# Performance work log

Measured on AMD Instinct MI355X. Metric: run time of the kernel, lower is better.

The kernel has to match this reference:

```python
import jax, jax.numpy as jnp
import numpy as np

NHEAD = 8; DM = 512; DFF = 2048; L = 4; S = 1024; NTOK = 51; MLP = 256; CLASSES = 7
GH = 3; GHID = 64; GCLS = 5; ALPHA = 0.2
HD = DM // NHEAD

_ADJ = np.array([[0,1,0,0,0],[1,1,1,1,0],[1,0,1,0,1],[1,0,0,1,1],[0,0,1,1,1]], dtype=np.int32)


def setup_inputs():
    key = jax.random.key(0)
    ks = jax.random.split(key, 24)
    r = lambda k, s, sc=0.05: jax.random.normal(k, s, jnp.float32) * sc
    return {
        'x': jax.random.normal(ks[0], (5, S, NTOK), jnp.float32),
        'adj': jnp.asarray(_ADJ),
        'W_enc': r(ks[1], (NTOK, DM)), 'b_enc': jnp.zeros((DM,), jnp.float32),
        'cls_tok': r(ks[2], (1, 1, DM)),
        'pos_emb': r(ks[3], (S + 1, DM)),
        'Wq': r(ks[4], (L, DM, DM)), 'bq': jnp.zeros((L, DM), jnp.float32),
        'Wk': r(ks[5], (L, DM, DM)), 'bk': jnp.zeros((L, DM), jnp.float32),
        'Wv': r(ks[6], (L, DM, DM)), 'bv': jnp.zeros((L, DM), jnp.float32),
        'Wo': r(ks[7], (L, DM, DM)), 'bo': jnp.zeros((L, DM), jnp.float32),
        'W1': r(ks[8], (L, DM, DFF)), 'b1': jnp.zeros((L, DFF), jnp.float32),
        'W2': r(ks[9], (L, DFF, DM)), 'b2': jnp.zeros((L, DM), jnp.float32),
        'g1': jnp.ones((L, DM), jnp.float32), 'be1': jnp.zeros((L, DM), jnp.float32),
        'g2': jnp.ones((L, DM), jnp.float32), 'be2': jnp.zeros((L, DM), jnp.float32),
        'Wd1': r(ks[10], (DM, MLP)), 'bd1': jnp.zeros((MLP,), jnp.float32),
        'Wd2': r(ks[11], (MLP, CLASSES)), 'bd2': jnp.zeros((CLASSES,), jnp.float32),
        'Wg': r(ks[12], (GH, 3, GHID), 0.3), 'ag': r(ks[13], (GH, 2 * GHID), 0.3),
        'Wgo': r(ks[14], (GH * GHID, GCLS), 0.3), 'ago': r(ks[15], (2 * GCLS,), 0.3),
    }


def _layernorm(x, g, b, eps=1e-5):
    m = x.mean(-1, keepdims=True)
    v = ((x - m) ** 2).mean(-1, keepdims=True)
    return (x - m) * jax.lax.rsqrt(v + eps) * g + b


def _gat_attn_layer(h_in, W, a, mask):
    # standard pyGAT GraphAttentionLayer: e_ij = LeakyReLU(a1.h_i + a2.h_j)
    F = W.shape[1]
    h = h_in @ W                                                    # [N, F]
    e = jax.nn.leaky_relu((h @ a[:F])[:, None] + (h @ a[F:])[None, :], ALPHA)
    att = jax.nn.softmax(jnp.where(mask, e, -9e15), axis=-1)        # adjacency-masked softmax
    return att @ h


def _gat(xg, mask, Wg, ag, Wgo, ago):
    # xg: [5 nodes, 3 feats]; GH attention heads concatenated, then output layer
    heads = jax.vmap(lambda W, a: jax.nn.elu(_gat_attn_layer(xg, W, a, mask)))(Wg, ag)  # [GH,5,GHID]
    hcat = jnp.transpose(heads, (1, 0, 2)).reshape(xg.shape[0], GH * GHID)
    out = jax.nn.elu(_gat_attn_layer(hcat, Wgo, ago, mask))         # [5, GCLS]
    return jax.nn.log_softmax(out, axis=1)


def _forward(x, adj, params):
    (W_enc, b_enc, cls_tok, pos_emb, Wq, bq, Wk, bk, Wv, bv, Wo, bo,
     W1, b1, W2, b2, g1, be1, g2, be2, Wd1, bd1, Wd2, bd2, Wg, ag, Wgo, ago) = params
    mask = adj > 0
    # --- batched GAT: the source loops over T timesteps x 5 feature groups; here fully vectorized ---
    # x[:, :, :15] : batch(=5 nodes) x T x 15 -> [T*5groups, 5 nodes, 3]
    xg = x[:, :, :15].reshape(5, S, 5, 3)
    xg = jnp.transpose(xg, (1, 2, 0, 3)).reshape(S * 5, 5, 3)
    gat_out = jax.vmap(lambda g: _gat(g, mask, Wg, ag, Wgo, ago))(xg)
    gat_out = gat_out.reshape(S, 5, 5, GCLS)                        # [T, group, node, class]
    # --- transformer branch (eval mode: dropout = identity) ---
    h = x @ W_enc + b_enc                                           # [5, S, DM]
    h = jnp.concatenate([jnp.broadcast_to(cls_tok, (5, 1, DM)), h], axis=1)
    h = h + pos_emb[None]
    for i in range(L):
        q = (h @ Wq[i] + bq[i]).reshape(5, S + 1, NHEAD, HD)
        k = (h @ Wk[i] + bk[i]).reshape(5, S + 1, NHEAD, HD)
        v = (h @ Wv[i] + bv[i]).reshape(5, S + 1, NHEAD, HD)
        sc = jnp.einsum('bthd,bshd->bhts', q, k) / jnp.sqrt(jnp.float32(HD))
        att = jax.nn.softmax(sc, axis=-1)
        o = jnp.einsum('bhts,bshd->bthd', att, v).reshape(5, S + 1, DM) @ Wo[i] + bo[i]
        h = _layernorm(h + o, g1[i], be1[i])
        f = jax.nn.relu(h @ W1[i] + b1[i]) @ W2[i] + b2[i]
        h = _layernorm(h + f, g2[i], be2[i])
    cls = h[:, 0, :]                                                # lambda: x[:, 0, :]
    out = (cls @ Wd1 + bd1) @ Wd2 + bd2                             # no activation between dense layers (as in source)
    return out, gat_out


def reference(x, adj, W_enc, b_enc, cls_tok, pos_emb, Wq, bq, Wk, bk, Wv, bv, Wo, bo, W1, b1, W2, b2, g1, be1, g2, be2, Wd1, bd1, Wd2, bd2, Wg, ag, Wgo, ago):
    params = (W_enc, b_enc, cls_tok, pos_emb, Wq, bq, Wk, bk, Wv, bv, Wo, bo,
              W1, b1, W2, b2, g1, be1, g2, be2, Wd1, bd1, Wd2, bd2, Wg, ag, Wgo, ago)
    return _forward(x, adj, params)
```

## Files before the change

### kernel.cpp

```cpp
#include <hip/hip_runtime.h>
#include <hip/hip_bf16.h>
#include <math.h>

#define NBATCH 5
#define SEQ    1024
#define T      1025
#define ROWS   (NBATCH * T)
#define MP     5248
#define DM     512
#define DFF    2048
#define NHEAD  8
#define HD     64
#define NTOK   51
#define MLPDIM 256
#define NCLS   7
#define GH     3
#define GHID   64
#define GCLS   5
#define NGRAPH (SEQ * 5)
#define QKVN   1536
#define TPAD   1088

typedef __attribute__((ext_vector_type(8))) short bf16x8;
typedef __attribute__((ext_vector_type(4))) float f32x4;

#define GM_AS(p)  ((const __attribute__((address_space(1))) void*)(p))
#define LDS_AS(p) ((__attribute__((address_space(3))) void*)(p))

__device__ __forceinline__ unsigned short f2bf(float f) {
    unsigned int u = __float_as_uint(f);
    unsigned int r = (u + 0x7FFFu + ((u >> 16) & 1u)) >> 16;
    return (unsigned short)r;
}
__device__ __forceinline__ float bf2f(unsigned short u) {
    return __uint_as_float((unsigned int)u << 16);
}

__global__ __launch_bounds__(256) void wconv_kernel(
    const float* __restrict__ W, unsigned short* __restrict__ Wt, int K, int N,
    long dstride)
{
    const float* Wm = W + (size_t)blockIdx.z * K * N;
    unsigned short* Wo = Wt + (size_t)blockIdx.z * dstride;
    __shared__ float tile[32][33];
    int bx = blockIdx.x * 32;
    int by = blockIdx.y * 32;
    int tx = threadIdx.x & 31, ty = threadIdx.x >> 5;
    #pragma unroll
    for (int i = 0; i < 32; i += 8)
        tile[ty + i][tx] = Wm[(size_t)(by + ty + i) * N + bx + tx];
    __syncthreads();
    #pragma unroll
    for (int i = 0; i < 32; i += 8)
        Wo[(size_t)(bx + ty + i) * K + by + tx] = f2bf(tile[tx][ty + i]);
}

__global__ __launch_bounds__(512) void bconcat_kernel(
    const float* __restrict__ bq, const float* __restrict__ bk,
    const float* __restrict__ bv, float* __restrict__ bqkv)
{
    int i = blockIdx.x, t = threadIdx.x;
    bqkv[i * QKVN + t]        = bq[i * DM + t];
    bqkv[i * QKVN + 512 + t]  = bk[i * DM + t];
    bqkv[i * QKVN + 1024 + t] = bv[i * DM + t];
}

__global__ __launch_bounds__(256) void gemm_mfma(
    const unsigned short* __restrict__ A, const unsigned short* __restrict__ Bt,
    const float* __restrict__ bias, float* __restrict__ Cf,
    unsigned short* __restrict__ Cb, int N, int K, int relu)
{
    __shared__ unsigned short As[128 * 64];
    __shared__ unsigned short Bs[128 * 64];
    int tid = threadIdx.x;
    int l = tid & 63, w = tid >> 6;
    int wr = w & 1, wc = w >> 1;
    int mlane = l & 15, quad = l >> 4;
    int m0 = blockIdx.y * 128, n0 = blockIdx.x * 128;

    f32x4 acc[4][4] = {};

    for (int k0 = 0; k0 < K; k0 += 64) {
        __syncthreads();
        #pragma unroll
        for (int it = 0; it < 4; ++it) {
            int c = tid + it * 256;
            int row = c >> 3, cc = c & 7;
            const unsigned short* ga = A  + (size_t)(m0 + row) * K + k0 + cc * 8;
            __builtin_amdgcn_global_load_lds(GM_AS(ga), LDS_AS(As + c * 8), 16, 0, 0);
            const unsigned short* gb = Bt + (size_t)(n0 + row) * K + k0 + cc * 8;
            __builtin_amdgcn_global_load_lds(GM_AS(gb), LDS_AS(Bs + c * 8), 16, 0, 0);
        }
        __syncthreads();
        #pragma unroll
        for (int half = 0; half < 2; ++half) {
            int ko = half * 32 + quad * 8;
            bf16x8 afrag[4], bfrag[4];
            #pragma unroll
            for (int mi = 0; mi < 4; ++mi)
                afrag[mi] = *(const bf16x8*)(As + (wr * 64 + mi * 16 + mlane) * 64 + ko);
            #pragma unroll
            for (int ni = 0; ni < 4; ++ni)
                bfrag[ni] = *(const bf16x8*)(Bs + (wc * 64 + ni * 16 + mlane) * 64 + ko);
            #pragma unroll
            for (int mi = 0; mi < 4; ++mi)
                #pragma unroll
                for (int ni = 0; ni < 4; ++ni)
                    acc[mi][ni] = __builtin_amdgcn_mfma_f32_16x16x32_bf16(
                        afrag[mi], bfrag[ni], acc[mi][ni], 0, 0, 0);
        }
    }

    #pragma unroll
    for (int mi = 0; mi < 4; ++mi) {
        #pragma unroll
        for (int r = 0; r < 4; ++r) {
            int gm = m0 + wr * 64 + mi * 16 + quad * 4 + r;
            size_t rowoff = (size_t)gm * N;
            #pragma unroll
            for (int ni = 0; ni < 4; ++ni) {
                int gn = n0 + wc * 64 + ni * 16 + mlane;
                float val = acc[mi][ni][r] + bias[gn];
                if (relu) val = fmaxf(val, 0.f);
                if (Cb) Cb[rowoff + gn] = f2bf(val);
                else    Cf[rowoff + gn] = val;
            }
        }
    }
}

__global__ __launch_bounds__(256) void gemm_mfma_sk(
    const unsigned short* __restrict__ A, const unsigned short* __restrict__ Bt,
    unsigned short* __restrict__ part, int N, int K)
{
    __shared__ unsigned short As[128 * 64];
    __shared__ unsigned short Bs[128 * 64];
    int tid = threadIdx.x;
    int l = tid & 63, w = tid >> 6;
    int wr = w & 1, wc = w >> 1;
    int mlane = l & 15, quad = l >> 4;
    int m0 = blockIdx.y * 128, n0 = blockIdx.x * 128;
    int kper = K / gridDim.z;
    int kbeg = blockIdx.z * kper;

    f32x4 acc[4][4] = {};

    for (int k0 = kbeg; k0 < kbeg + kper; k0 += 64) {
        __syncthreads();
        #pragma unroll
        for (int it = 0; it < 4; ++it) {
            int c = tid + it * 256;
            int row = c >> 3, cc = c & 7;
            const unsigned short* ga = A  + (size_t)(m0 + row) * K + k0 + cc * 8;
            __builtin_amdgcn_global_load_lds(GM_AS(ga), LDS_AS(As + c * 8), 16, 0, 0);
            const unsigned short* gb = Bt + (size_t)(n0 + row) * K + k0 + cc * 8;
            __builtin_amdgcn_global_load_lds(GM_AS(gb), LDS_AS(Bs + c * 8), 16, 0, 0);
        }
        __syncthreads();
        #pragma unroll
        for (int half = 0; half < 2; ++half) {
            int ko = half * 32 + quad * 8;
            bf16x8 afrag[4], bfrag[4];
            #pragma unroll
            for (int mi = 0; mi < 4; ++mi)
                afrag[mi] = *(const bf16x8*)(As + (wr * 64 + mi * 16 + mlane) * 64 + ko);
            #pragma unroll
            for (int ni = 0; ni < 4; ++ni)
                bfrag[ni] = *(const bf16x8*)(Bs + (wc * 64 + ni * 16 + mlane) * 64 + ko);
            #pragma unroll
            for (int mi = 0; mi < 4; ++mi)
                #pragma unroll
                for (int ni = 0; ni < 4; ++ni)
                    acc[mi][ni] = __builtin_amdgcn_mfma_f32_16x16x32_bf16(
                        afrag[mi], bfrag[ni], acc[mi][ni], 0, 0, 0);
        }
    }

    unsigned short* pz = part + (size_t)blockIdx.z * MP * N;
    #pragma unroll
    for (int mi = 0; mi < 4; ++mi) {
        #pragma unroll
        for (int r = 0; r < 4; ++r) {
            int gm = m0 + wr * 64 + mi * 16 + quad * 4 + r;
            size_t rowoff = (size_t)gm * N;
            #pragma unroll
            for (int ni = 0; ni < 4; ++ni) {
                int gn = n0 + wc * 64 + ni * 16 + mlane;
                pz[rowoff + gn] = f2bf(acc[mi][ni][r]);
            }
        }
    }
}

__global__ __launch_bounds__(256) void vtrans_kernel(
    const unsigned short* __restrict__ vb, unsigned short* __restrict__ vt, int qs)
{
    __shared__ unsigned short tile[64][72];
    int bh = blockIdx.y;
    int b = bh >> 3, h = bh & 7;
    int t0 = blockIdx.x * 64;
    int tid = threadIdx.x;
    #pragma unroll
    for (int it = 0; it < 2; ++it) {
        int c = tid + it * 256;
        int key = c >> 3, cc = c & 7;
        int gk = t0 + key; if (gk >= T) gk = T - 1;
        *(bf16x8*)(&tile[key][cc * 8]) =
            *(const bf16x8*)(vb + ((size_t)b * T + gk) * qs + h * HD + cc * 8);
    }
    __syncthreads();
    #pragma unroll
    for (int it = 0; it < 2; ++it) {
        int c = tid + it * 256;
        int d = c >> 3, cc = c & 7;
        unsigned short tmp[8];
        #pragma unroll
        for (int j = 0; j < 8; ++j) tmp[j] = tile[cc * 8 + j][d];
        *(bf16x8*)(vt + ((size_t)bh * 64 + d) * TPAD + t0 + cc * 8) = *(bf16x8*)tmp;
    }
}

#define AQT 64
#define NCH 17
__global__ __launch_bounds__(256) void attn_mfma(
    const unsigned short* __restrict__ qb, const unsigned short* __restrict__ kb,
    const unsigned short* __restrict__ vt, unsigned short* __restrict__ ob,
    int qs)
{
    __shared__ unsigned short Ks[64 * 72];
    __shared__ unsigned short Vs[64 * 72];
    __shared__ unsigned short Ps[4][16 * 72];
    int bh = blockIdx.y;
    int b = bh >> 3, h = bh & 7;
    int t0 = blockIdx.x * AQT;
    int tid = threadIdx.x;
    int l = tid & 63, w = tid >> 6;
    int ml = l & 15, quad = l >> 4;
    size_t rowbase = (size_t)b * T;
    const unsigned short* vtb = vt + (size_t)bh * 64 * TPAD;

    int qrow = t0 + w * 16 + ml; if (qrow >= T) qrow = T - 1;
    const unsigned short* qp = qb + (rowbase + qrow) * qs + h * HD + quad * 8;
    bf16x8 qf0 = *(const bf16x8*)qp;
    bf16x8 qf1 = *(const bf16x8*)(qp + 32);

    int rowa = tid >> 3, cca = tid & 7;
    int rowb = (tid + 256) >> 3, ccb = tid & 7;

    f32x4 oacc[4] = {};
    float lrow[4] = {0.f, 0.f, 0.f, 0.f};

    bf16x8 kra, krb, vra, vrb;
    {
        kra = *(const bf16x8*)(kb + (rowbase + rowa) * qs + h * HD + cca * 8);
        krb = *(const bf16x8*)(kb + (rowbase + rowb) * qs + h * HD + ccb * 8);
        vra = *(const bf16x8*)(vtb + (size_t)rowa * TPAD + cca * 8);
        vrb = *(const bf16x8*)(vtb + (size_t)rowb * TPAD + ccb * 8);
    }

    for (int ch = 0; ch < NCH; ++ch) {
        int c0 = ch * 64;
        __syncthreads();
        *(bf16x8*)(Ks + rowa * 72 + cca * 8) = kra;
        *(bf16x8*)(Ks + rowb * 72 + ccb * 8) = krb;
        *(bf16x8*)(Vs + rowa * 72 + cca * 8) = vra;
        *(bf16x8*)(Vs + rowb * 72 + ccb * 8) = vrb;
        __syncthreads();
        if (ch + 1 < NCH) {
            int n0k = c0 + 64;
            int gka = n0k + rowa; if (gka >= T) gka = T - 1;
            int gkb = n0k + rowb; if (gkb >= T) gkb = T - 1;
            kra = *(const bf16x8*)(kb + (rowbase + gka) * qs + h * HD + cca * 8);
            krb = *(const bf16x8*)(kb + (rowbase + gkb) * qs + h * HD + ccb * 8);
            vra = *(const bf16x8*)(vtb + (size_t)rowa * TPAD + n0k + cca * 8);
            vrb = *(const bf16x8*)(vtb + (size_t)rowb * TPAD + n0k + ccb * 8);
        }

        f32x4 s[4] = {};
        #pragma unroll
        for (int ni = 0; ni < 4; ++ni) {
            bf16x8 kf0 = *(const bf16x8*)(Ks + (ni * 16 + ml) * 72 + quad * 8);
            bf16x8 kf1 = *(const bf16x8*)(Ks + (ni * 16 + ml) * 72 + 32 + quad * 8);
            s[ni] = __builtin_amdgcn_mfma_f32_16x16x32_bf16(qf0, kf0, s[ni], 0, 0, 0);
            s[ni] = __builtin_amdgcn_mfma_f32_16x16x32_bf16(qf1, kf1, s[ni], 0, 0, 0);
        }
        #pragma unroll
        for (int ni = 0; ni < 4; ++ni) {
            bool valid = (c0 + ni * 16 + ml) < T;
            #pragma unroll
            for (int r = 0; r < 4; ++r) {
                float p = valid ? __expf(s[ni][r] * 0.125f) : 0.f;
                s[ni][r] = p;
                lrow[r] += p;
            }
        }
        unsigned short* pw = Ps[w];
        #pragma unroll
        for (int r = 0; r < 4; ++r)
            #pragma unroll
            for (int ni = 0; ni < 4; ++ni)
                pw[(quad * 4 + r) * 72 + ((ni * 16 + ml) ^ (quad << 4))] = f2bf(s[ni][r]);
        int sw = ((ml >> 2) & 3) << 4;
        #pragma unroll
        for (int kc = 0; kc < 2; ++kc) {
            bf16x8 pf = *(const bf16x8*)(pw + ml * 72 + ((kc * 32 + quad * 8) ^ sw));
            #pragma unroll
            for (int ni = 0; ni < 4; ++ni) {
                bf16x8 vf = *(const bf16x8*)(Vs + (ni * 16 + ml) * 72 + kc * 32 + quad * 8);
                oacc[ni] = __builtin_amdgcn_mfma_f32_16x16x32_bf16(pf, vf, oacc[ni], 0, 0, 0);
            }
        }
    }

    #pragma unroll
    for (int r = 0; r < 4; ++r) {
        #pragma unroll
        for (int off = 1; off < 16; off <<= 1)
            lrow[r] += __shfl_xor(lrow[r], off);
    }
    #pragma unroll
    for (int r = 0; r < 4; ++r) {
        int grow = t0 + w * 16 + quad * 4 + r;
        if (grow >= T) continue;
        float inv = 1.f / lrow[r];
        unsigned short* op = ob + (rowbase + grow) * DM + h * HD;
        #pragma unroll
        for (int ni = 0; ni < 4; ++ni)
            op[ni * 16 + ml] = f2bf(oacc[ni][r] * inv);
    }
}

__global__ __launch_bounds__(256) void encoder_kernel(
    const float* __restrict__ x, const float* __restrict__ W_enc,
    const float* __restrict__ b_enc, const float* __restrict__ cls_tok,
    const float* __restrict__ pos_emb, float* __restrict__ h,
    unsigned short* __restrict__ hb)
{
    int row = blockIdx.x;
    int b = row / T, tt = row % T;
    int tid = threadIdx.x;
    float* hp = h + (size_t)row * DM;
    unsigned short* hbp = hb + (size_t)row * DM;
    if (tt == 0) {
        float a0 = cls_tok[tid]       + pos_emb[tid];
        float a1 = cls_tok[tid + 256] + pos_emb[tid + 256];
        hp[tid] = a0; hp[tid + 256] = a1;
        hbp[tid] = f2bf(a0); hbp[tid + 256] = f2bf(a1);
        return;
    }
    __shared__ float xs[NTOK];
    int s = tt - 1;
    if (tid < NTOK) xs[tid] = x[((size_t)b * SEQ + s) * NTOK + tid];
    __syncthreads();
    #pragma unroll
    for (int rep = 0; rep < 2; ++rep) {
        int d = tid + rep * 256;
        float acc = b_enc[d] + pos_emb[(size_t)tt * DM + d];
        for (int kx = 0; kx < NTOK; ++kx) acc += xs[kx] * W_enc[kx * DM + d];
        hp[d] = acc;
        hbp[d] = f2bf(acc);
    }
}

__global__ __launch_bounds__(256) void add_lnp_kernel(
    float* __restrict__ h, const unsigned short* __restrict__ part, int np,
    const float* __restrict__ bias, const float* __restrict__ g,
    const float* __restrict__ be, unsigned short* __restrict__ hb)
{
    int w = threadIdx.x >> 6, l = threadIdx.x & 63;
    int row = blockIdx.x * 4 + w;
    if (row >= ROWS) return;
    float* hp = h + (size_t)row * DM + l * 8;
    unsigned short* hbp = hb + (size_t)row * DM + l * 8;
    float4 a0 = *(const float4*)(hp);
    float4 a1 = *(const float4*)(hp + 4);
    float4 b0 = *(const float4*)(bias + l * 8);
    float4 b1 = *(const float4*)(bias + l * 8 + 4);
    float v[8] = {a0.x + b0.x, a0.y + b0.y, a0.z + b0.z, a0.w + b0.w,
                  a1.x + b1.x, a1.y + b1.y, a1.z + b1.z, a1.w + b1.w};
    for (int pp = 0; pp < np; ++pp) {
        const unsigned short* prp = part + ((size_t)pp * MP + row) * DM + l * 8;
        bf16x8 pv = *(const bf16x8*)prp;
        #pragma unroll
        for (int i = 0; i < 8; ++i) v[i] += bf2f((unsigned short)pv[i]);
    }
    float s = 0.f;
    #pragma unroll
    for (int i = 0; i < 8; ++i) s += v[i];
    #pragma unroll
    for (int off = 1; off < 64; off <<= 1) s += __shfl_xor(s, off);
    float mean = s * (1.f / DM);
    float sq = 0.f;
    #pragma unroll
    for (int i = 0; i < 8; ++i) { v[i] -= mean; sq += v[i] * v[i]; }
    #pragma unroll
    for (int off = 1; off < 64; off <<= 1) sq += __shfl_xor(sq, off);
    float inv = rsqrtf(sq * (1.f / DM) + 1e-5f);
    float4 g0 = *(const float4*)(g + l * 8);
    float4 g1 = *(const float4*)(g + l * 8 + 4);
    float4 e0 = *(const float4*)(be + l * 8);
    float4 e1 = *(const float4*)(be + l * 8 + 4);
    float o[8];
    o[0] = v[0]*inv*g0.x + e0.x; o[1] = v[1]*inv*g0.y + e0.y;
    o[2] = v[2]*inv*g0.z + e0.z; o[3] = v[3]*inv*g0.w + e0.w;
    o[4] = v[4]*inv*g1.x + e1.x; o[5] = v[5]*inv*g1.y + e1.y;
    o[6] = v[6]*inv*g1.z + e1.z; o[7] = v[7]*inv*g1.w + e1.w;
    *(float4*)(hp)     = make_float4(o[0], o[1], o[2], o[3]);
    *(float4*)(hp + 4) = make_float4(o[4], o[5], o[6], o[7]);
    ushort4 p0 = {f2bf(o[0]), f2bf(o[1]), f2bf(o[2]), f2bf(o[3])};
    ushort4 p1 = {f2bf(o[4]), f2bf(o[5]), f2bf(o[6]), f2bf(o[7])};
    *(ushort4*)(hbp)     = p0;
    *(ushort4*)(hbp + 4) = p1;
}

__global__ __launch_bounds__(256) void dec1_kernel(
    const float* __restrict__ h, const float* __restrict__ Wd1,
    float* __restrict__ part)
{
    int kc = blockIdx.x, b = blockIdx.y, tid = threadIdx.x;
    __shared__ float cs[64];
    const float* cls = h + (size_t)b * T * DM;
    if (tid < 64) cs[tid] = cls[kc * 64 + tid];
    __syncthreads();
    float acc = 0.f;
    #pragma unroll
    for (int kx = 0; kx < 64; ++kx)
        acc += cs[kx] * Wd1[(size_t)(kc * 64 + kx) * MLPDIM + tid];
    part[(size_t)(b * 8 + kc) * MLPDIM + tid] = acc;
}

__global__ __launch_bounds__(256) void dec2_kernel(
    const float* __restrict__ part, const float* __restrict__ bd1,
    const float* __restrict__ Wd2, const float* __restrict__ bd2,
    float* __restrict__ out)
{
    __shared__ float t1s[MLPDIM];
    int tid = threadIdx.x;
    for (int b = 0; b < NBATCH; ++b) {
        float acc = bd1[tid];
        #pragma unroll
        for (int kc = 0; kc < 8; ++kc)
            acc += part[(size_t)(b * 8 + kc) * MLPDIM + tid];
        t1s[tid] = acc;
        __syncthreads();
        if (tid < NCLS) {
            float a2 = bd2[tid];
            for (int kx = 0; kx < MLPDIM; ++kx) a2 += t1s[kx] * Wd2[kx * NCLS + tid];
            out[b * NCLS + tid] = a2;
        }
        __syncthreads();
    }
}

__global__ __launch_bounds__(64) void gat_kernel(
    const float* __restrict__ x, const int* __restrict__ adj,
    const float* __restrict__ Wg, const float* __restrict__ ag,
    const float* __restrict__ Wgo, const float* __restrict__ ago,
    float* __restrict__ out)
{
    int g = blockIdx.x;
    int s = g / 5, jj = g % 5;
    int tid = threadIdx.x;
    __shared__ float xs[5][3];
    __shared__ int adjs[25];
    __shared__ float hb[GH][5][GHID];
    __shared__ float o1[GH][5][GHID];
    __shared__ float srcb[GH][5], dstb[GH][5];
    __shared__ float attb[GH][5][5];
    __shared__ float h2[5][5], src2[5], dst2[5], att2[5][5], o2[5][5];

    if (tid < 15) { int n = tid / 3, c = tid % 3;
        xs[n][c] = x[(size_t)n * SEQ * NTOK + (size_t)s * NTOK + jj * 3 + c]; }
    if (tid < 25) adjs[tid] = adj[tid];
    __syncthreads();

    #pragma unroll
    for (int hh = 0; hh < GH; ++hh)
        #pragma unroll
        for (int n = 0; n < 5; ++n)
            hb[hh][n][tid] = xs[n][0] * Wg[hh * 192 + tid]
                           + xs[n][1] * Wg[hh * 192 + 64 + tid]
                           + xs[n][2] * Wg[hh * 192 + 128 + tid];
    __syncthreads();

    if (tid < 15) { int hh = tid / 5, n = tid % 5; float a = 0.f;
        for (int f = 0; f < GHID; ++f) a += hb[hh][n][f] * ag[hh * 128 + f];
        srcb[hh][n] = a;
    } else if (tid >= 32 && tid < 47) { int t2 = tid - 32; int hh = t2 / 5, n = t2 % 5; float a = 0.f;
        for (int f = 0; f < GHID; ++f) a += hb[hh][n][f] * ag[hh * 128 + 64 + f];
        dstb[hh][n] = a;
    }
    __syncthreads();

    if (tid < 15) { int hh = tid / 5, i = tid % 5;
        float e[5]; float mx = -1e30f;
        #pragma unroll
        for (int j2 = 0; j2 < 5; ++j2) {
            float ev = srcb[hh][i] + dstb[hh][j2];
            ev = ev > 0.f ? ev : 0.2f * ev;
            e[j2] = ev;
            if (adjs[i * 5 + j2] && ev > mx) mx = ev;
        }
        float sum = 0.f;
        #pragma unroll
        for (int j2 = 0; j2 < 5; ++j2) {
            float p = adjs[i * 5 + j2] ? expf(e[j2] - mx) : 0.f;
            e[j2] = p; sum += p;
        }
        float inv = 1.f / sum;
        #pragma unroll
        for (int j2 = 0; j2 < 5; ++j2) attb[hh][i][j2] = e[j2] * inv;
    }
    __syncthreads();

    #pragma unroll
    for (int hh = 0; hh < GH; ++hh)
        #pragma unroll
        for (int n = 0; n < 5; ++n) {
            float a = 0.f;
            #pragma unroll
            for (int j2 = 0; j2 < 5; ++j2) a += attb[hh][n][j2] * hb[hh][j2][tid];
            o1[hh][n][tid] = a > 0.f ? a : expm1f(a);
        }
    __syncthreads();

    if (tid < 25) { int n = tid / 5, m = tid % 5; float a = 0.f;
        for (int hh = 0; hh < GH; ++hh)
            for (int f = 0; f < GHID; ++f)
                a += o1[hh][n][f] * Wgo[(hh * GHID + f) * GCLS + m];
        h2[n][m] = a;
    }
    __syncthreads();

    if (tid < 5) { float a = 0.f;
        for (int m = 0; m < GCLS; ++m) a += h2[tid][m] * ago[m];
        src2[tid] = a;
    } else if (tid >= 8 && tid < 13) { int n = tid - 8; float a = 0.f;
        for (int m = 0; m < GCLS; ++m) a += h2[n][m] * ago[GCLS + m];
        dst2[n] = a;
    }
    __syncthreads();

    if (tid < 5) { int i = tid;
        float e[5]; float mx = -1e30f;
        #pragma unroll
        for (int j2 = 0; j2 < 5; ++j2) {
            float ev = src2[i] + dst2[j2];
            ev = ev > 0.f ? ev : 0.2f * ev;
            e[j2] = ev;
            if (adjs[i * 5 + j2] && ev > mx) mx = ev;
        }
        float sum = 0.f;
        #pragma unroll
        for (int j2 = 0; j2 < 5; ++j2) {
            float p = adjs[i * 5 + j2] ? expf(e[j2] - mx) : 0.f;
            e[j2] = p; sum += p;
        }
        float inv = 1.f / sum;
        #pragma unroll
        for (int j2 = 0; j2 < 5; ++j2) att2[i][j2] = e[j2] * inv;
    }
    __syncthreads();

    if (tid < 25) { int n = tid / 5, m = tid % 5; float a = 0.f;
        #pragma unroll
        for (int j2 = 0; j2 < 5; ++j2) a += att2[n][j2] * h2[j2][m];
        o2[n][m] = a > 0.f ? a : expm1f(a);
    }
    __syncthreads();

    if (tid < 5) { int n = tid;
        float mx = o2[n][0];
        #pragma unroll
        for (int m = 1; m < GCLS; ++m) mx = fmaxf(mx, o2[n][m]);
        float sum = 0.f;
        #pragma unroll
        for (int m = 0; m < GCLS; ++m) sum += expf(o2[n][m] - mx);
        float ls = logf(sum);
        #pragma unroll
        for (int m = 0; m < GCLS; ++m)
            out[(size_t)g * 25 + n * 5 + m] = o2[n][m] - mx - ls;
    }
}

extern "C" void kernel_launch(void* const* d_in, const int* in_sizes, int n_in,
                              void* d_out, int out_size, void* d_ws, size_t ws_size,
                              hipStream_t stream)
{
    const float* x       = (const float*)d_in[0];
    const int*   adj     = (const int*)  d_in[1];
    const float* W_enc   = (const float*)d_in[2];
    const float* b_enc   = (const float*)d_in[3];
    const float* cls_tok = (const float*)d_in[4];
    const float* pos_emb = (const float*)d_in[5];
    const float* Wq = (const float*)d_in[6];
    const float* bq = (const float*)d_in[7];
    const float* Wk = (const float*)d_in[8];
    const float* bk = (const float*)d_in[9];
    const float* Wv = (const float*)d_in[10];
    const float* bv = (const float*)d_in[11];
    const float* Wo = (const float*)d_in[12];
    const float* bo = (const float*)d_in[13];
    const float* W1 = (const float*)d_in[14];
    const float* b1 = (const float*)d_in[15];
    const float* W2 = (const float*)d_in[16];
    const float* b2 = (const float*)d_in[17];
    const float* g1 = (const float*)d_in[18];
    const float* be1= (const float*)d_in[19];
    const float* g2 = (const float*)d_in[20];
    const float* be2= (const float*)d_in[21];
    const float* Wd1= (const float*)d_in[22];
    const float* bd1= (const float*)d_in[23];
    const float* Wd2= (const float*)d_in[24];
    const float* bd2= (const float*)d_in[25];
    const float* Wg = (const float*)d_in[26];
    const float* ag = (const float*)d_in[27];
    const float* Wgo= (const float*)d_in[28];
    const float* ago= (const float*)d_in[29];
    float* out = (float*)d_out;

    float* ws = (float*)d_ws;
    float* h = ws;
    unsigned short* hb   = (unsigned short*)(h + (size_t)MP * DM);
    unsigned short* qkvb = hb + (size_t)MP * DM;
    unsigned short* ob   = qkvb + (size_t)MP * QKVN;
    unsigned short* f1b  = qkvb;
    unsigned short* Wqkvt= ob + (size_t)MP * DM;
    unsigned short* Wot  = Wqkvt + (size_t)4 * QKVN * DM;
    unsigned short* W1t  = Wot + (size_t)4 * DM * DM;
    unsigned short* W2t  = W1t + (size_t)4 * DM * DFF;
    float* bqkv = (float*)(W2t + (size_t)4 * DFF * DM);
    float* dpart = bqkv + 4 * QKVN;
    unsigned short* vt = (unsigned short*)(dpart + NBATCH * 8 * MLPDIM);
    unsigned short* parts = vt + (size_t)40 * 64 * TPAD;

    const long QS = (long)QKVN * DM;
    wconv_kernel<<<dim3(DM/32,  DM/32,  4), 256, 0, stream>>>(Wq, Wqkvt,            DM,  DM, QS);
    wconv_kernel<<<dim3(DM/32,  DM/32,  4), 256, 0, stream>>>(Wk, Wqkvt + 512*512,  DM,  DM, QS);
    wconv_kernel<<<dim3(DM/32,  DM/32,  4), 256, 0, stream>>>(Wv, Wqkvt + 1024*512, DM,  DM, QS);
    wconv_kernel<<<dim3(DM/32,  DM/32,  4), 256, 0, stream>>>(Wo, Wot, DM,  DM, (long)DM*DM);
    wconv_kernel<<<dim3(DFF/32, DM/32,  4), 256, 0, stream>>>(W1, W1t, DM,  DFF, (long)DM*DFF);
    wconv_kernel<<<dim3(DM/32,  DFF/32, 4), 256, 0, stream>>>(W2, W2t, DFF, DM, (long)DFF*DM);
    bconcat_kernel<<<4, 512, 0, stream>>>(bq, bk, bv, bqkv);

    gat_kernel<<<NGRAPH, 64, 0, stream>>>(x, adj, Wg, ag, Wgo, ago, out + NBATCH * NCLS);
    encoder_kernel<<<ROWS, 256, 0, stream>>>(x, W_enc, b_enc, cls_tok, pos_emb, h, hb);

    dim3 gqkv (QKVN / 128, MP / 128);
    dim3 g2048(DFF / 128, MP / 128);
    dim3 gWo  (DM / 128, MP / 128, 2);
    dim3 gW2  (DM / 128, MP / 128, 4);
    dim3 gAttn(TPAD / AQT, NBATCH * NHEAD);
    dim3 gVt  (TPAD / 64, NBATCH * NHEAD);
    int gLN = (ROWS + 3) / 4;

    for (int i = 0; i < 4; ++i) {
        gemm_mfma<<<gqkv, 256, 0, stream>>>(hb, Wqkvt + (size_t)i*QKVN*DM, bqkv + i*QKVN, nullptr, qkvb, QKVN, DM, 0);
        vtrans_kernel<<<gVt, 256, 0, stream>>>(qkvb + 1024, vt, QKVN);
        attn_mfma<<<gAttn, 256, 0, stream>>>(qkvb, qkvb + 512, vt, ob, QKVN);
        gemm_mfma_sk<<<gWo, 256, 0, stream>>>(ob, Wot + (size_t)i*DM*DM, parts, DM, DM);
        add_lnp_kernel<<<gLN, 256, 0, stream>>>(h, parts, 2, bo + i*DM, g1 + i*DM, be1 + i*DM, hb);
        gemm_mfma<<<g2048, 256, 0, stream>>>(hb,  W1t + (size_t)i*DM*DFF, b1 + i*DFF, nullptr, f1b, DFF, DM, 1);
        gemm_mfma_sk<<<gW2, 256, 0, stream>>>(f1b, W2t + (size_t)i*DM*DFF, parts, DM, DFF);
        add_lnp_kernel<<<gLN, 256, 0, stream>>>(h, parts, 4, b2 + i*DM, g2 + i*DM, be2 + i*DM, hb);
    }

    dec1_kernel<<<dim3(8, NBATCH), 256, 0, stream>>>(h, Wd1, dpart);
    dec2_kernel<<<1, 256, 0, stream>>>(dpart, bd1, Wd2, bd2, out);
}
```

Measured before the change: 824.4 us.

## Process 128 keys per attention round and fuse weight-conversion launches

The attention kernel now stages 128 keys and values per shared-memory round instead of 64, halving the number of barrier-separated rounds and prefetch steps. V transpose padding grows to cover the larger chunk. The separate per-weight conversion and bias concatenation launches are merged into a single setup kernel to cut launch overhead. LDS use and register pressure per attention block increase, which may reduce occupancy.

```diff
diff --git a/kernel.cpp b/kernel.cpp
--- a/kernel.cpp
+++ b/kernel.cpp
@@ -19,7 +19,7 @@
 #define GCLS   5
 #define NGRAPH (SEQ * 5)
 #define QKVN   1536
-#define TPAD   1088
+#define TPAD   1152
 
 typedef __attribute__((ext_vector_type(8))) short bf16x8;
 typedef __attribute__((ext_vector_type(4))) float f32x4;
@@ -36,33 +36,59 @@
     return __uint_as_float((unsigned int)u << 16);
 }
 
-__global__ __launch_bounds__(256) void wconv_kernel(
-    const float* __restrict__ W, unsigned short* __restrict__ Wt, int K, int N,
-    long dstride)
-{
-    const float* Wm = W + (size_t)blockIdx.z * K * N;
-    unsigned short* Wo = Wt + (size_t)blockIdx.z * dstride;
+__global__ __launch_bounds__(256) void setup_kernel(
+    const float* __restrict__ Wq, const float* __restrict__ Wk,
+    const float* __restrict__ Wv, const float* __restrict__ Wo_,
+    const float* __restrict__ W1, const float* __restrict__ W2,
+    const float* __restrict__ bq, const float* __restrict__ bk,
+    const float* __restrict__ bv,
+    unsigned short* __restrict__ Wqkvt, unsigned short* __restrict__ Wot,
+    unsigned short* __restrict__ W1t, unsigned short* __restrict__ W2t,
+    float* __restrict__ bqkv)
+{
+    int id = blockIdx.x;
+    if (id >= 12288) {
+        int i = id - 12288;
+        #pragma unroll
+        for (int rep = 0; rep < 2; ++rep) {
+            int t = threadIdx.x + rep * 256;
+            bqkv[i * QKVN + t]        = bq[i * DM + t];
+            bqkv[i * QKVN + 512 + t]  = bk[i * DM + t];
+            bqkv[i * QKVN + 1024 + t] = bv[i * DM + t];
+        }
+        return;
+    }
+    const float* W; unsigned short* Wt; int K, N, z, bx, by; long dstride;
+    if (id < 4096) {
+        int g = id >> 10, lid = id & 1023;
+        K = DM; N = DM;
+        z = lid >> 8; int r2 = lid & 255; by = r2 >> 4; bx = r2 & 15;
+        if (g < 3) { W = (g == 0) ? Wq : (g == 1) ? Wk : Wv;
+                     Wt = Wqkvt + (size_t)g * DM * DM; dstride = (long)QKVN * DM; }
+        else       { W = Wo_; Wt = Wot; dstride = (long)DM * DM; }
+    } else if (id < 8192) {
+        int lid = id - 4096;
+        K = DM; N = DFF;
+        z = lid >> 10; int r2 = lid & 1023; by = r2 >> 6; bx = r2 & 63;
+        W = W1; Wt = W1t; dstride = (long)DM * DFF;
+    } else {
+        int lid = id - 8192;
+        K = DFF; N = DM;
+        z = lid >> 10; int r2 = lid & 1023; by = r2 >> 4; bx = r2 & 15;
+        W = W2; Wt = W2t; dstride = (long)DFF * DM;
+    }
+    const float* Wm = W + (size_t)z * K * N;
+    unsigned short* Wo2 = Wt + (size_t)z * dstride;
     __shared__ float tile[32][33];
-    int bx = blockIdx.x * 32;
-    int by = blockIdx.y * 32;
+    int bX = bx * 32, bY = by * 32;
     int tx = threadIdx.x & 31, ty = threadIdx.x >> 5;
     #pragma unroll
     for (int i = 0; i < 32; i += 8)
-        tile[ty + i][tx] = Wm[(size_t)(by + ty + i) * N + bx + tx];
+        tile[ty + i][tx] = Wm[(size_t)(bY + ty + i) * N + bX + tx];
     __syncthreads();
     #pragma unroll
     for (int i = 0; i < 32; i += 8)
-        Wo[(size_t)(bx + ty + i) * K + by + tx] = f2bf(tile[tx][ty + i]);
-}
-
-__global__ __launch_bounds__(512) void bconcat_kernel(
-    const float* __restrict__ bq, const float* __restrict__ bk,
-    const float* __restrict__ bv, float* __restrict__ bqkv)
-{
-    int i = blockIdx.x, t = threadIdx.x;
-    bqkv[i * QKVN + t]        = bq[i * DM + t];
-    bqkv[i * QKVN + 512 + t]  = bk[i * DM + t];
-    bqkv[i * QKVN + 1024 + t] = bv[i * DM + t];
+        Wo2[(size_t)(bX + ty + i) * K + bY + tx] = f2bf(tile[tx][ty + i]);
 }
 
 __global__ __launch_bounds__(256) void gemm_mfma(
@@ -221,14 +247,14 @@
 }
 
 #define AQT 64
-#define NCH 17
+#define NR 9
 __global__ __launch_bounds__(256) void attn_mfma(
     const unsigned short* __restrict__ qb, const unsigned short* __restrict__ kb,
     const unsigned short* __restrict__ vt, unsigned short* __restrict__ ob,
     int qs)
 {
-    __shared__ unsigned short Ks[64 * 72];
-    __shared__ unsigned short Vs[64 * 72];
+    __shared__ unsigned short Ks[128 * 72];
+    __shared__ unsigned short Vs[64 * 136];
     __shared__ unsigned short Ps[4][16 * 72];
     int bh = blockIdx.y;
     int b = bh >> 3, h = bh & 7;
@@ -244,70 +270,76 @@
     bf16x8 qf0 = *(const bf16x8*)qp;
     bf16x8 qf1 = *(const bf16x8*)(qp + 32);
 
-    int rowa = tid >> 3, cca = tid & 7;
-    int rowb = (tid + 256) >> 3, ccb = tid & 7;
+    int krow = tid >> 3, kcc = tid & 7;
+    int vd   = tid >> 4, vck = tid & 15;
 
     f32x4 oacc[4] = {};
     float lrow[4] = {0.f, 0.f, 0.f, 0.f};
 
-    bf16x8 kra, krb, vra, vrb;
-    {
-        kra = *(const bf16x8*)(kb + (rowbase + rowa) * qs + h * HD + cca * 8);
-        krb = *(const bf16x8*)(kb + (rowbase + rowb) * qs + h * HD + ccb * 8);
-        vra = *(const bf16x8*)(vtb + (size_t)rowa * TPAD + cca * 8);
-        vrb = *(const bf16x8*)(vtb + (size_t)rowb * TPAD + ccb * 8);
-    }
-
-    for (int ch = 0; ch < NCH; ++ch) {
-        int c0 = ch * 64;
-        __syncthreads();
-        *(bf16x8*)(Ks + rowa * 72 + cca * 8) = kra;
-        *(bf16x8*)(Ks + rowb * 72 + ccb * 8) = krb;
-        *(bf16x8*)(Vs + rowa * 72 + cca * 8) = vra;
-        *(bf16x8*)(Vs + rowb * 72 + ccb * 8) = vrb;
-        __syncthreads();
-        if (ch + 1 < NCH) {
-            int n0k = c0 + 64;
-            int gka = n0k + rowa; if (gka >= T) gka = T - 1;
-            int gkb = n0k + rowb; if (gkb >= T) gkb = T - 1;
-            kra = *(const bf16x8*)(kb + (rowbase + gka) * qs + h * HD + cca * 8);
-            krb = *(const bf16x8*)(kb + (rowbase + gkb) * qs + h * HD + ccb * 8);
-            vra = *(const bf16x8*)(vtb + (size_t)rowa * TPAD + n0k + cca * 8);
-            vrb = *(const bf16x8*)(vtb + (size_t)rowb * TPAD + n0k + ccb * 8);
-        }
-
-        f32x4 s[4] = {};
-        #pragma unroll
-        for (int ni = 0; ni < 4; ++ni) {
-            bf16x8 kf0 = *(const bf16x8*)(Ks + (ni * 16 + ml) * 72 + quad * 8);
-            bf16x8 kf1 = *(const bf16x8*)(Ks + (ni * 16 + ml) * 72 + 32 + quad * 8);
-            s[ni] = __builtin_amdgcn_mfma_f32_16x16x32_bf16(qf0, kf0, s[ni], 0, 0, 0);
-            s[ni] = __builtin_amdgcn_mfma_f32_16x16x32_bf16(qf1, kf1, s[ni], 0, 0, 0);
-        }
-        #pragma unroll
-        for (int ni = 0; ni < 4; ++ni) {
-            bool valid = (c0 + ni * 16 + ml) < T;
-            #pragma unroll
-            for (int r = 0; r < 4; ++r) {
-                float p = valid ? __expf(s[ni][r] * 0.125f) : 0.f;
-                s[ni][r] = p;
-                lrow[r] += p;
+    bf16x8 kr[4], vr[4];
+    #pragma unroll
+    for (int i = 0; i < 4; ++i) {
+        int gk = krow + i * 32; if (gk >= T) gk = T - 1;
+        kr[i] = *(const bf16x8*)(kb + (rowbase + gk) * qs + h * HD + kcc * 8);
+        vr[i] = *(const bf16x8*)(vtb + (size_t)(vd + i * 16) * TPAD + vck * 8);
+    }
+
+    for (int rnd = 0; rnd < NR; ++rnd) {
+        int c0 = rnd * 128;
+        __syncthreads();
+        #pragma unroll
+        for (int i = 0; i < 4; ++i) {
+            *(bf16x8*)(Ks + (krow + i * 32) * 72 + kcc * 8) = kr[i];
+            *(bf16x8*)(Vs + (vd + i * 16) * 136 + vck * 8) = vr[i];
+        }
+        __syncthreads();
+        if (rnd + 1 < NR) {
+            int n0k = c0 + 128;
+            #pragma unroll
+            for (int i = 0; i < 4; ++i) {
+                int gk = n0k + krow + i * 32; if (gk >= T) gk = T - 1;
+                kr[i] = *(const bf16x8*)(kb + (rowbase + gk) * qs + h * HD + kcc * 8);
+                vr[i] = *(const bf16x8*)(vtb + (size_t)(vd + i * 16) * TPAD + n0k + vck * 8);
             }
         }
-        unsigned short* pw = Ps[w];
-        #pragma unroll
-        for (int r = 0; r < 4; ++r)
-            #pragma unroll
-            for (int ni = 0; ni < 4; ++ni)
-                pw[(quad * 4 + r) * 72 + ((ni * 16 + ml) ^ (quad << 4))] = f2bf(s[ni][r]);
-        int sw = ((ml >> 2) & 3) << 4;
-        #pragma unroll
-        for (int kc = 0; kc < 2; ++kc) {
-            bf16x8 pf = *(const bf16x8*)(pw + ml * 72 + ((kc * 32 + quad * 8) ^ sw));
+
+        #pragma unroll
+        for (int p = 0; p < 2; ++p) {
+            int kb0 = p * 64;
+            f32x4 s[4] = {};
             #pragma unroll
             for (int ni = 0; ni < 4; ++ni) {
-                bf16x8 vf = *(const bf16x8*)(Vs + (ni * 16 + ml) * 72 + kc * 32 + quad * 8);
-                oacc[ni] = __builtin_amdgcn_mfma_f32_16x16x32_bf16(pf, vf, oacc[ni], 0, 0, 0);
+                const unsigned short* kfp = Ks + (kb0 + ni * 16 + ml) * 72 + quad * 8;
+                bf16x8 kf0 = *(const bf16x8*)kfp;
+                bf16x8 kf1 = *(const bf16x8*)(kfp + 32);
+                s[ni] = __builtin_amdgcn_mfma_f32_16x16x32_bf16(qf0, kf0, s[ni], 0, 0, 0);
+                s[ni] = __builtin_amdgcn_mfma_f32_16x16x32_bf16(qf1, kf1, s[ni], 0, 0, 0);
+            }
+            #pragma unroll
+            for (int ni = 0; ni < 4; ++ni) {
+                bool valid = (c0 + kb0 + ni * 16 + ml) < T;
+                #pragma unroll
+                for (int r = 0; r < 4; ++r) {
+                    float pv = valid ? __expf(s[ni][r] * 0.125f) : 0.f;
+                    s[ni][r] = pv;
+                    lrow[r] += pv;
+                }
+            }
+            unsigned short* pw = Ps[w];
+            #pragma unroll
+            for (int r = 0; r < 4; ++r)
+                #pragma unroll
+                for (int ni = 0; ni < 4; ++ni)
+                    pw[(quad * 4 + r) * 72 + ((ni * 16 + ml) ^ (quad << 4))] = f2bf(s[ni][r]);
+            int sw = ((ml >> 2) & 3) << 4;
+            #pragma unroll
+            for (int kc = 0; kc < 2; ++kc) {
+                bf16x8 pf = *(const bf16x8*)(pw + ml * 72 + ((kc * 32 + quad * 8) ^ sw));
+                #pragma unroll
+                for (int ni = 0; ni < 4; ++ni) {
+                    bf16x8 vf = *(const bf16x8*)(Vs + (ni * 16 + ml) * 136 + kb0 + kc * 32 + quad * 8);
+                    oacc[ni] = __builtin_amdgcn_mfma_f32_16x16x32_bf16(pf, vf, oacc[ni], 0, 0, 0);
+                }
             }
         }
     }
@@ -634,14 +666,8 @@
     unsigned short* vt = (unsigned short*)(dpart + NBATCH * 8 * MLPDIM);
     unsigned short* parts = vt + (size_t)40 * 64 * TPAD;
 
-    const long QS = (long)QKVN * DM;
-    wconv_kernel<<<dim3(DM/32,  DM/32,  4), 256, 0, stream>>>(Wq, Wqkvt,            DM,  DM, QS);
-    wconv_kernel<<<dim3(DM/32,  DM/32,  4), 256, 0, stream>>>(Wk, Wqkvt + 512*512,  DM,  DM, QS);
-    wconv_kernel<<<dim3(DM/32,  DM/32,  4), 256, 0, stream>>>(Wv, Wqkvt + 1024*512, DM,  DM, QS);
-    wconv_kernel<<<dim3(DM/32,  DM/32,  4), 256, 0, stream>>>(Wo, Wot, DM,  DM, (long)DM*DM);
-    wconv_kernel<<<dim3(DFF/32, DM/32,  4), 256, 0, stream>>>(W1, W1t, DM,  DFF, (long)DM*DFF);
-    wconv_kernel<<<dim3(DM/32,  DFF/32, 4), 256, 0, stream>>>(W2, W2t, DFF, DM, (long)DFF*DM);
-    bconcat_kernel<<<4, 512, 0, stream>>>(bq, bk, bv, bqkv);
+    setup_kernel<<<12292, 256, 0, stream>>>(Wq, Wk, Wv, Wo, W1, W2, bq, bk, bv,
+                                            Wqkvt, Wot, W1t, W2t, bqkv);
 
     gat_kernel<<<NGRAPH, 64, 0, stream>>>(x, adj, Wg, ag, Wgo, ago, out + NBATCH * NCLS);
     encoder_kernel<<<ROWS, 256, 0, stream>>>(x, W_enc, b_enc, cls_tok, pos_emb, h, hb);
@@ -650,7 +676,7 @@
     dim3 g2048(DFF / 128, MP / 128);
     dim3 gWo  (DM / 128, MP / 128, 2);
     dim3 gW2  (DM / 128, MP / 128, 4);
-    dim3 gAttn(TPAD / AQT, NBATCH * NHEAD);
+    dim3 gAttn(17, NBATCH * NHEAD);
     dim3 gVt  (TPAD / 64, NBATCH * NHEAD);
     int gLN = (ROWS + 3) / 4;
 
```

Result: faster. 798.8 us (-3.1%).
